# Kernel tuning notes

Hardware: AMD Instinct MI355X
Metric: run time of the kernel (lower is better)

Reference implementation:

```python
import jax, jax.numpy as jnp
import numpy as np

B, T, C = 2, 2048, 1024
H = 16
DH = C // H  # 64
DFF = 4 * C  # 4096
EPS = 1e-5


def layernorm(x, gamma, beta):
    # torch.var defaults to unbiased (ddof=1) -- replicate exactly
    m = jnp.mean(x, axis=-1, keepdims=True)
    v = jnp.var(x, axis=-1, ddof=1, keepdims=True)
    return (x - m) / jnp.sqrt(v + EPS) * gamma + beta


def setup_inputs() -> dict:
    key = jax.random.key(0)
    ks = jax.random.split(key, 12)
    s = 0.02
    return {
        "x": jax.random.normal(ks[0], (B, T, C), jnp.float32),
        "Wq": jax.random.normal(ks[1], (H, C, DH), jnp.float32) * s,
        "bq": jnp.zeros((H, DH), jnp.float32),
        "Wk": jax.random.normal(ks[2], (H, C, DH), jnp.float32) * s,
        "bk": jnp.zeros((H, DH), jnp.float32),
        "Wv": jax.random.normal(ks[3], (H, C, DH), jnp.float32) * s,
        "bv": jnp.zeros((H, DH), jnp.float32),
        "Wo": jax.random.normal(ks[4], (C, C), jnp.float32) * s,
        "bo": jnp.zeros((C,), jnp.float32),
        "gamma1": jnp.ones((C,), jnp.float32),
        "beta1": jnp.zeros((C,), jnp.float32),
        "gamma2": jnp.ones((C,), jnp.float32),
        "beta2": jnp.zeros((C,), jnp.float32),
        "W1": jax.random.normal(ks[5], (C, DFF), jnp.float32) * s,
        "b1": jnp.zeros((DFF,), jnp.float32),
        "W2": jax.random.normal(ks[6], (DFF, C), jnp.float32) * s,
        "b2": jnp.zeros((C,), jnp.float32),
    }


def reference(x, Wq, bq, Wk, bk, Wv, bv, Wo, bo,
              gamma1, beta1, gamma2, beta2, W1, b1, W2, b2):
    Tn = x.shape[1]
    # Block: x = ln1(x); x = x + attn(x); x = ln2(x); out = x + ffw(x)
    x = layernorm(x, gamma1, beta1)

    # per-head Q/K/V linears, stacked over heads: [B,T,C] x [H,C,Dh] -> [B,H,T,Dh]
    q = jnp.einsum('btc,hcd->bhtd', x, Wq) + bq[None, :, None, :]
    k = jnp.einsum('btc,hcd->bhtd', x, Wk) + bk[None, :, None, :]
    v = jnp.einsum('btc,hcd->bhtd', x, Wv) + bv[None, :, None, :]

    scale = DH ** -0.5
    scores = jnp.einsum('bhtd,bhsd->bhts', q, k) * scale  # [B,H,T,T]
    causal = jnp.tril(jnp.ones((Tn, Tn), dtype=bool))
    scores = jnp.where(causal, scores, -jnp.inf)
    alpha = jax.nn.softmax(scores, axis=-1)
    h = jnp.einsum('bhts,bhsd->bhtd', alpha, v)  # [B,H,T,Dh]
    h = jnp.transpose(h, (0, 2, 1, 3)).reshape(x.shape)  # concat heads -> [B,T,C]
    attn_out = h @ Wo + bo

    x = x + attn_out
    x = layernorm(x, gamma2, beta2)
    ffw = jax.nn.gelu(x @ W1 + b1, approximate=False) @ W2 + b2
    return x + ffw
```

## Files before the change

kernel.cpp:

```cpp
#include <hip/hip_runtime.h>

typedef unsigned short u16;
typedef unsigned int u32;
typedef __attribute__((ext_vector_type(8))) short bf16x8;
typedef __attribute__((ext_vector_type(4))) float f32x4;

#define AS1 __attribute__((address_space(1)))
#define AS3 __attribute__((address_space(3)))

__device__ __forceinline__ u16 f2bf(float f) {
  u32 u = __float_as_uint(f);
  u = (u + 0x7fffu + ((u >> 16) & 1u)) >> 16;
  return (u16)u;
}
__device__ __forceinline__ float bf2f(u16 v) { return __uint_as_float((u32)v << 16); }

__device__ __forceinline__ void gl16(const void* g, void* l) {
  __builtin_amdgcn_global_load_lds((AS1 void*)g, (AS3 void*)l, 16, 0, 0);
}

__device__ __forceinline__ float exp2a(float x) {
  float r;
  asm("v_exp_f32 %0, %1" : "=v"(r) : "v"(x));
  return r;
}
__device__ __forceinline__ u32 pk2(float lo, float hi) {
  u32 r;
  asm("v_cvt_pk_bf16_f32 %0, %1, %2" : "=v"(r) : "v"(lo), "v"(hi));
  return r;
}

#define BAR() __builtin_amdgcn_s_barrier()
#define LGKM0()                                         \
  do {                                                  \
    asm volatile("s_waitcnt lgkmcnt(0)" ::: "memory");  \
    __builtin_amdgcn_sched_barrier(0);                  \
  } while (0)
#define VMC0()                                          \
  do {                                                  \
    asm volatile("s_waitcnt vmcnt(0)" ::: "memory");    \
    __builtin_amdgcn_sched_barrier(0);                  \
  } while (0)

__global__ __launch_bounds__(256) void ln_kernel(const float* __restrict__ in,
                                                 const float* __restrict__ gamma,
                                                 const float* __restrict__ beta,
                                                 u16* __restrict__ obf,
                                                 float* __restrict__ of32) {
  const int row = blockIdx.x;
  const int tid = threadIdx.x;
  const float* xr = in + (long)row * 1024;
  float4 v = *(const float4*)(xr + tid * 4);
  float s = v.x + v.y + v.z + v.w;
  float sq = v.x * v.x + v.y * v.y + v.z * v.z + v.w * v.w;
#pragma unroll
  for (int off = 1; off < 64; off <<= 1) {
    s += __shfl_xor(s, off);
    sq += __shfl_xor(sq, off);
  }
  __shared__ float rs[4], rq[4];
  const int w = tid >> 6, lane = tid & 63;
  if (lane == 0) { rs[w] = s; rq[w] = sq; }
  __syncthreads();
  s = rs[0] + rs[1] + rs[2] + rs[3];
  sq = rq[0] + rq[1] + rq[2] + rq[3];
  const float mean = s * (1.0f / 1024.0f);
  const float var = (sq - 1024.0f * mean * mean) * (1.0f / 1023.0f);
  const float rstd = rsqrtf(var + 1e-5f);
  float4 g4 = *(const float4*)(gamma + tid * 4);
  float4 b4 = *(const float4*)(beta + tid * 4);
  float o0 = (v.x - mean) * rstd * g4.x + b4.x;
  float o1 = (v.y - mean) * rstd * g4.y + b4.y;
  float o2 = (v.z - mean) * rstd * g4.z + b4.z;
  float o3 = (v.w - mean) * rstd * g4.w + b4.w;
  *(float4*)(of32 + (long)row * 1024 + tid * 4) = make_float4(o0, o1, o2, o3);
  ushort4 ub;
  ub.x = f2bf(o0); ub.y = f2bf(o1); ub.z = f2bf(o2); ub.w = f2bf(o3);
  *(ushort4*)(obf + (long)row * 1024 + tid * 4) = ub;
}

__global__ __launch_bounds__(256) void ln2_fused_kernel(
    const u16* __restrict__ p0, const u16* __restrict__ p1,
    const float* __restrict__ bo, const float* __restrict__ xn,
    const float* __restrict__ gamma, const float* __restrict__ beta,
    u16* __restrict__ obf, float* __restrict__ of32) {
  const int row = blockIdx.x;
  const int tid = threadIdx.x;
  const long i4 = (long)row * 1024 + tid * 4;
  ushort4 a0 = *(const ushort4*)(p0 + i4);
  ushort4 a1 = *(const ushort4*)(p1 + i4);
  float4 xv = *(const float4*)(xn + i4);
  float4 bv = *(const float4*)(bo + tid * 4);
  float y0 = bf2f(a0.x) + bf2f(a1.x) + bv.x + xv.x;
  float y1 = bf2f(a0.y) + bf2f(a1.y) + bv.y + xv.y;
  float y2 = bf2f(a0.z) + bf2f(a1.z) + bv.z + xv.z;
  float y3 = bf2f(a0.w) + bf2f(a1.w) + bv.w + xv.w;
  float s = y0 + y1 + y2 + y3;
  float sq = y0 * y0 + y1 * y1 + y2 * y2 + y3 * y3;
#pragma unroll
  for (int off = 1; off < 64; off <<= 1) {
    s += __shfl_xor(s, off);
    sq += __shfl_xor(sq, off);
  }
  __shared__ float rs[4], rq[4];
  const int w = tid >> 6, lane = tid & 63;
  if (lane == 0) { rs[w] = s; rq[w] = sq; }
  __syncthreads();
  s = rs[0] + rs[1] + rs[2] + rs[3];
  sq = rq[0] + rq[1] + rq[2] + rq[3];
  const float mean = s * (1.0f / 1024.0f);
  const float var = (sq - 1024.0f * mean * mean) * (1.0f / 1023.0f);
  const float rstd = rsqrtf(var + 1e-5f);
  float4 g4 = *(const float4*)(gamma + tid * 4);
  float4 b4 = *(const float4*)(beta + tid * 4);
  float o0 = (y0 - mean) * rstd * g4.x + b4.x;
  float o1 = (y1 - mean) * rstd * g4.y + b4.y;
  float o2 = (y2 - mean) * rstd * g4.z + b4.z;
  float o3 = (y3 - mean) * rstd * g4.w + b4.w;
  *(float4*)(of32 + i4) = make_float4(o0, o1, o2, o3);
  ushort4 ub;
  ub.x = f2bf(o0); ub.y = f2bf(o1); ub.z = f2bf(o2); ub.w = f2bf(o3);
  *(ushort4*)(obf + i4) = ub;
}

__global__ __launch_bounds__(256) void wtrans_kernel(const float* __restrict__ in,
                                                     u16* __restrict__ out,
                                                     int R, int C, int in_rs,
                                                     long in_batch, long out_batch) {
  __shared__ float tile[32][33];
  const float* ip = in + (long)blockIdx.z * in_batch;
  u16* op = out + (long)blockIdx.z * out_batch;
  const int c0 = blockIdx.x * 32, r0 = blockIdx.y * 32;
  const int tx = threadIdx.x, ty = threadIdx.y;
#pragma unroll
  for (int i = 0; i < 4; ++i)
    tile[ty + i * 8][tx] = ip[(long)(r0 + ty + i * 8) * in_rs + c0 + tx];
  __syncthreads();
#pragma unroll
  for (int i = 0; i < 4; ++i)
    op[(long)(c0 + ty + i * 8) * R + r0 + tx] = f2bf(tile[tx][ty + i * 8]);
}

__device__ __forceinline__ void mfma_phase(f32x4 acc[8][4], const bf16x8 af[4][2],
                                           const bf16x8 bf[2][2], int mq, int nq) {
#pragma unroll
  for (int mf = 0; mf < 4; ++mf)
#pragma unroll
    for (int nf = 0; nf < 2; ++nf)
#pragma unroll
      for (int kh = 0; kh < 2; ++kh)
        acc[mq * 4 + mf][nq * 2 + nf] = __builtin_amdgcn_mfma_f32_16x16x32_bf16(
            af[mf][kh], bf[nf][kh], acc[mq * 4 + mf][nq * 2 + nf], 0, 0, 0);
}

#define STGA(BUFX)                                          \
  do {                                                      \
    gl16(pA0, Asm + (BUFX) * 16384 + tid * 8);              \
    gl16(pA1, Asm + (BUFX) * 16384 + 4096 + tid * 8);       \
    gl16(pA2, Asm + (BUFX) * 16384 + 8192 + tid * 8);       \
    gl16(pA3, Asm + (BUFX) * 16384 + 12288 + tid * 8);      \
  } while (0)
#define STGB(BUFX)                                          \
  do {                                                      \
    gl16(pB0, Bsm + (BUFX) * 16384 + tid * 8);              \
    gl16(pB1, Bsm + (BUFX) * 16384 + 4096 + tid * 8);       \
    gl16(pB2, Bsm + (BUFX) * 16384 + 8192 + tid * 8);       \
    gl16(pB3, Bsm + (BUFX) * 16384 + 12288 + tid * 8);      \
  } while (0)
#define ADVA() do { pA0 += 64; pA1 += 64; pA2 += 64; pA3 += 64; } while (0)
#define ADVB() do { pB0 += 64; pB1 += 64; pB2 += 64; pB3 += 64; } while (0)

#define RD(arr, off) (*(const bf16x8*)((arr) + (off)))

#define KTILE2(BUF, T)                                                       \
  do {                                                                       \
    bf16x8 af[4][2], bv0[2][2], bv1[2][2];                                   \
    _Pragma("unroll") for (int mf = 0; mf < 4; ++mf)                         \
        _Pragma("unroll") for (int kh = 0; kh < 2; ++kh)                     \
            af[mf][kh] = RD(Asm, aO[mf][kh] + (BUF) * 16384);                \
    _Pragma("unroll") for (int nf = 0; nf < 2; ++nf)                         \
        _Pragma("unroll") for (int kh = 0; kh < 2; ++kh) {                   \
      bv0[nf][kh] = RD(Bsm, bO[nf][kh] + (BUF) * 16384);                     \
      bv1[nf][kh] = RD(Bsm, bO[nf][kh] + (BUF) * 16384 + 2048);              \
    }                                                                        \
    if ((T) + 1 < nk) { STGA((BUF) ^ 1); STGB((BUF) ^ 1); }                  \
    LGKM0();                                                                 \
    mfma_phase(acc, af, bv0, 0, 0);                                          \
    mfma_phase(acc, af, bv1, 0, 1);                                          \
    _Pragma("unroll") for (int mf = 0; mf < 4; ++mf)                         \
        _Pragma("unroll") for (int kh = 0; kh < 2; ++kh)                     \
            af[mf][kh] = RD(Asm, aO[mf][kh] + (BUF) * 16384 + 4096);         \
    LGKM0();                                                                 \
    mfma_phase(acc, af, bv0, 1, 0);                                          \
    mfma_phase(acc, af, bv1, 1, 1);                                          \
    if ((T) + 1 < nk) VMC0();                                                \
    BAR();                                                                   \
  } while (0)

template <int EPI>
__global__ __launch_bounds__(512, 2) void gemm8_kernel(
    const u16* __restrict__ A, const u16* __restrict__ Bt,
    int lda, int ldb, int M, int N, int nk,
    const float* bias0, const float* bias1, const float* bias2,
    void* out0, void* out1) {
  __shared__ __align__(16) u16 Asm[4 * 8192];
  __shared__ __align__(16) u16 Bsm[4 * 8192];
  const int tid = threadIdx.x;
  const int lane = tid & 63, w = tid >> 6;
  const int wm = w >> 2, wn = w & 3;
  const int q15 = lane & 15, g = lane >> 4;

  const int nbx = gridDim.x, nby = gridDim.y;
  const int nwg = nbx * nby * gridDim.z;
  int lid = blockIdx.x + nbx * (blockIdx.y + nby * blockIdx.z);
  lid = (lid & 7) * (nwg >> 3) + (lid >> 3);
  const int bx = lid % nbx;
  const int rest = lid / nbx;
  const int by = rest % nby;
  const int bz = rest / nby;

  const long m0 = (long)bx * 256;
  const long n0 = (long)by * 256;
  const long koff = (long)bz * (long)nk * 64;
  const u16* Ab = A + m0 * lda + koff;
  const u16* Bb = Bt + n0 * ldb + koff;

  const int jr = tid >> 3;
  const int js = ((tid & 7) ^ (jr & 7)) * 8;
  const u16* pA0 = Ab + (long)jr * lda + js;
  const u16* pA1 = pA0 + (long)64 * lda;
  const u16* pA2 = pA0 + (long)128 * lda;
  const u16* pA3 = pA0 + (long)192 * lda;
  const u16* pB0 = Bb + (long)jr * ldb + js;
  const u16* pB1 = pB0 + (long)64 * ldb;
  const u16* pB2 = pB0 + (long)128 * ldb;
  const u16* pB3 = pB0 + (long)192 * ldb;

  int aO[4][2], bO[2][2];
#pragma unroll
  for (int mf = 0; mf < 4; ++mf)
#pragma unroll
    for (int kh = 0; kh < 2; ++kh) {
      const int rh = mf * 16 + q15;
      aO[mf][kh] = wm * 8192 + rh * 64 + (((kh * 4 + g) ^ (rh & 7)) * 8);
    }
  const int brow = (wn & 1) * 64;
#pragma unroll
  for (int nf = 0; nf < 2; ++nf)
#pragma unroll
    for (int kh = 0; kh < 2; ++kh) {
      const int rh = brow + nf * 16 + q15;
      bO[nf][kh] = (wn >> 1) * 8192 + rh * 64 + (((kh * 4 + g) ^ (rh & 7)) * 8);
    }

  f32x4 acc[8][4];
  f32x4 zero4 = {0.f, 0.f, 0.f, 0.f};
#pragma unroll
  for (int mi = 0; mi < 8; ++mi)
#pragma unroll
    for (int ni = 0; ni < 4; ++ni) acc[mi][ni] = zero4;

  STGA(0);
  STGB(0);
  ADVA();
  ADVB();
  VMC0();
  BAR();

  for (int tt = 0; tt < nk; tt += 2) {
    KTILE2(0, tt);
    ADVA(); ADVB();
    KTILE2(1, tt + 1);
    ADVA(); ADVB();
  }

#pragma unroll
  for (int mi = 0; mi < 8; ++mi) {
#pragma unroll
    for (int ni = 0; ni < 4; ++ni) {
      const long mbase = m0 + wm * 128 + (mi >> 2) * 64 + (mi & 3) * 16 + 4 * g;
      const long n = n0 + wn * 64 + (ni >> 1) * 32 + (ni & 1) * 16 + q15;
      f32x4 a = acc[mi][ni];
      if constexpr (EPI == 0) {
        const int sel = (int)(n >> 10);
        const int nn = (int)(n & 1023);
        const float* bp = sel == 0 ? bias0 : (sel == 1 ? bias1 : bias2);
        const float bb2 = bp[nn];
        if (sel < 2) {
          const float sc = (sel == 0) ? 0.18033688011112043f : 1.0f;
          u16* qkp = (u16*)out0;
#pragma unroll
          for (int r = 0; r < 4; ++r)
            qkp[(mbase + r) * 2048 + n] = f2bf((a[r] + bb2) * sc);
        } else {
          const int bI = (int)(mbase >> 11);
          const int t = (int)(mbase & 2047);
          const int hh = nn >> 6, dh = nn & 63;
          ushort4 pk;
          pk.x = f2bf(a[0] + bb2); pk.y = f2bf(a[1] + bb2);
          pk.z = f2bf(a[2] + bb2); pk.w = f2bf(a[3] + bb2);
          *(ushort4*)((u16*)out1 + ((long)((bI * 16 + hh) * 64 + dh)) * 2048 + t) = pk;
        }
      } else if constexpr (EPI == 2) {
        u16* gp = (u16*)out0;
        const float bb2 = bias0[(int)n];
#pragma unroll
        for (int r = 0; r < 4; ++r) {
          const float xg = a[r] + bb2;
          const float ge = 0.5f * xg * (1.0f + erff(xg * 0.70710678118f));
          gp[(mbase + r) * N + n] = f2bf(ge);
        }
      } else {
        u16* pp = (u16*)out0 + (long)bz * M * N;
#pragma unroll
        for (int r = 0; r < 4; ++r) pp[(mbase + r) * N + n] = f2bf(a[r]);
      }
    }
  }
}

__global__ __launch_bounds__(256) void ffn2_reduce_kernel(const u16* __restrict__ p,
                                                          const float* __restrict__ b2,
                                                          const float* __restrict__ yn,
                                                          float* __restrict__ out) {
  const long i4 = ((long)blockIdx.x * 256 + threadIdx.x) * 4;
  ushort4 p0 = *(const ushort4*)(p + i4);
  ushort4 p1 = *(const ushort4*)(p + 4194304 + i4);
  ushort4 p2 = *(const ushort4*)(p + 8388608 + i4);
  ushort4 p3 = *(const ushort4*)(p + 12582912 + i4);
  float4 rr = *(const float4*)(yn + i4);
  const int nn = (int)(i4 & 1023);
  float4 bb = *(const float4*)(b2 + nn);
  float4 o;
  o.x = bf2f(p0.x) + bf2f(p1.x) + bf2f(p2.x) + bf2f(p3.x) + bb.x + rr.x;
  o.y = bf2f(p0.y) + bf2f(p1.y) + bf2f(p2.y) + bf2f(p3.y) + bb.y + rr.y;
  o.z = bf2f(p0.z) + bf2f(p1.z) + bf2f(p2.z) + bf2f(p3.z) + bb.z + rr.z;
  o.w = bf2f(p0.w) + bf2f(p1.w) + bf2f(p2.w) + bf2f(p3.w) + bb.w + rr.w;
  *(float4*)(out + i4) = o;
}

__global__ __launch_bounds__(256, 2) void gemm_wo_kernel(const u16* __restrict__ A,
                                                         const u16* __restrict__ Bt,
                                                         u16* __restrict__ part) {
  __shared__ __align__(16) u16 Asm[128 * 64];
  __shared__ __align__(16) u16 Bsm[128 * 64];
  const int tid = threadIdx.x;
  const int lane = tid & 63, w = tid >> 6;
  const int wm = w >> 1, wn = w & 1;
  const int q = lane & 15, g = lane >> 4;
  const long m0 = (long)blockIdx.x * 128;
  const long n0 = (long)blockIdx.y * 128;
  const int bz = blockIdx.z;
  const long koff = (long)bz * 512;

  f32x4 zero4 = {0.f, 0.f, 0.f, 0.f};
  f32x4 acc[4][4];
#pragma unroll
  for (int mi = 0; mi < 4; ++mi)
#pragma unroll
    for (int ni = 0; ni < 4; ++ni) acc[mi][ni] = zero4;

  for (int ks = 0; ks < 8; ++ks) {
    __syncthreads();
    const u16* ga = A + m0 * 1024 + koff + ks * 64;
    const u16* gb = Bt + n0 * 1024 + koff + ks * 64;
    const int base = w * 256;
#pragma unroll
    for (int i = 0; i < 4; ++i) {
      const int idx = base + i * 64 + lane;
      const int row = idx >> 3;
      const int lg = (idx & 7) ^ (row & 7);
      gl16(ga + (long)row * 1024 + lg * 8, Asm + (long)(base + i * 64) * 8);
    }
#pragma unroll
    for (int i = 0; i < 4; ++i) {
      const int idx = base + i * 64 + lane;
      const int row = idx >> 3;
      const int lg = (idx & 7) ^ (row & 7);
      gl16(gb + (long)row * 1024 + lg * 8, Bsm + (long)(base + i * 64) * 8);
    }
    __syncthreads();
#pragma unroll
    for (int half = 0; half < 2; ++half) {
      bf16x8 af[4], bfv[4];
#pragma unroll
      for (int mi = 0; mi < 4; ++mi) {
        const int row = wm * 64 + mi * 16 + q;
        const int ph = (half * 4 + g) ^ (row & 7);
        af[mi] = *(const bf16x8*)(Asm + row * 64 + ph * 8);
      }
#pragma unroll
      for (int ni = 0; ni < 4; ++ni) {
        const int row = wn * 64 + ni * 16 + q;
        const int ph = (half * 4 + g) ^ (row & 7);
        bfv[ni] = *(const bf16x8*)(Bsm + row * 64 + ph * 8);
      }
#pragma unroll
      for (int mi = 0; mi < 4; ++mi)
#pragma unroll
        for (int ni = 0; ni < 4; ++ni)
          acc[mi][ni] = __builtin_amdgcn_mfma_f32_16x16x32_bf16(af[mi], bfv[ni],
                                                                acc[mi][ni], 0, 0, 0);
    }
  }
  u16* pp = part + (long)bz * 4096 * 1024;
#pragma unroll
  for (int mi = 0; mi < 4; ++mi) {
#pragma unroll
    for (int ni = 0; ni < 4; ++ni) {
      const long mbase = m0 + wm * 64 + mi * 16 + 4 * g;
      const long n = n0 + wn * 64 + ni * 16 + q;
      f32x4 a = acc[mi][ni];
#pragma unroll
      for (int r = 0; r < 4; ++r) pp[(mbase + r) * 1024 + n] = f2bf(a[r]);
    }
  }
}

__device__ __forceinline__ void attn_stage(const u16* kbase, const u16* vtb, int kb,
                                           u16* Kd, u16* Vd, int tid) {
#pragma unroll
  for (int it = 0; it < 2; ++it) {
    const int j = it * 256 + tid;
    const int row = j >> 3;
    const int lg = (j & 7) ^ (row & 7);
    gl16(kbase + (long)(kb * 64 + row) * 2048 + lg * 8, Kd + j * 8);
    gl16(vtb + (long)row * 2048 + kb * 64 + lg * 8, Vd + j * 8);
  }
}

__device__ __forceinline__ void softmax_slab(const f32x4 st[4], bool diag, int qrow,
                                             int kb, int g, int q15,
                                             float& m2, float& l, u16* prow,
                                             float al[4]) {
  float sv[4][4];
  float rmax = -1e30f;
#pragma unroll
  for (int sub = 0; sub < 4; ++sub)
#pragma unroll
    for (int r = 0; r < 4; ++r) {
      float s_ = st[sub][r];
      if (diag) {
        const int key = kb * 64 + sub * 16 + 4 * g + r;
        s_ = (key > qrow) ? -1e30f : s_;
      }
      sv[sub][r] = s_;
      rmax = fmaxf(rmax, s_);
    }
  rmax = fmaxf(rmax, __shfl_xor(rmax, 16));
  rmax = fmaxf(rmax, __shfl_xor(rmax, 32));
  const float mnew = fmaxf(m2, rmax);
  const float alpha = exp2a(m2 - mnew);
  float psum = 0.f;
#pragma unroll
  for (int sub = 0; sub < 4; ++sub) {
    const float p0 = exp2a(sv[sub][0] - mnew);
    const float p1 = exp2a(sv[sub][1] - mnew);
    const float p2 = exp2a(sv[sub][2] - mnew);
    const float p3 = exp2a(sv[sub][3] - mnew);
    uint2 u;
    u.x = pk2(p0, p1);
    u.y = pk2(p2, p3);
    *(uint2*)(prow + sub * 16 + 4 * g) = u;
    psum += (p0 + p1) + (p2 + p3);
  }
  psum += __shfl_xor(psum, 16);
  psum += __shfl_xor(psum, 32);
  l = l * alpha + psum;
  m2 = mnew;
#pragma unroll
  for (int r = 0; r < 4; ++r) al[r] = __shfl(alpha, 4 * g + r);
}

__global__ __launch_bounds__(256, 2) void attn_kernel(const u16* __restrict__ qk,
                                                      const u16* __restrict__ vT,
                                                      u16* __restrict__ o) {
  __shared__ __align__(16) u16 Ksm[2][64 * 64];
  __shared__ __align__(16) u16 Vsm[2][64 * 64];
  __shared__ __align__(16) u16 Psm[8][16][72];
  const int lid = blockIdx.x;
  const int xcd = lid & 7, s6 = lid >> 3;
  const int b2 = (s6 >> 4) & 3, xr = s6 & 15;
  const int qs = (b2 & 2) ? (15 - xr) : xr;
  const int bh = xcd + 8 * b2;
  const int b = bh >> 4, h = bh & 15;
  const int tid = threadIdx.x, lane = tid & 63, w = tid >> 6;
  const int q15 = lane & 15, g = lane >> 4;
  const u16* qbase = qk + (long)b * 2048 * 2048 + h * 64;
  const u16* kbase = qbase + 1024;
  const u16* vtb = vT + (long)bh * 64 * 2048;
  f32x4 zero4 = {0.f, 0.f, 0.f, 0.f};

  const int r0 = qs * 128 + w * 16 + q15;
  bf16x8 qa[2][2];
  qa[0][0] = *(const bf16x8*)(qbase + (long)r0 * 2048 + g * 8);
  qa[0][1] = *(const bf16x8*)(qbase + (long)r0 * 2048 + 32 + g * 8);
  qa[1][0] = *(const bf16x8*)(qbase + (long)(r0 + 64) * 2048 + g * 8);
  qa[1][1] = *(const bf16x8*)(qbase + (long)(r0 + 64) * 2048 + 32 + g * 8);

  f32x4 oa0[4], oa1[4];
#pragma unroll
  for (int dv = 0; dv < 4; ++dv) { oa0[dv] = zero4; oa1[dv] = zero4; }
  float m20 = -1e30f, l0 = 0.f, m21 = -1e30f, l1 = 0.f;
  const int kbmax = 2 * qs + 1;

  attn_stage(kbase, vtb, 0, Ksm[0], Vsm[0], tid);
  VMC0();
  __syncthreads();

  for (int kb = 0; kb <= kbmax; ++kb) {
    const int buf = kb & 1;
    if (kb < kbmax) attn_stage(kbase, vtb, kb + 1, Ksm[buf ^ 1], Vsm[buf ^ 1], tid);
    const u16* Kb = Ksm[buf];
    const u16* Vb = Vsm[buf];
    const bool s0on = (kb <= 2 * qs);
    f32x4 st0[4], st1[4];
#pragma unroll
    for (int sub = 0; sub < 4; ++sub) {
      const int row = sub * 16 + q15;
      const bf16x8 ka0 = *(const bf16x8*)(Kb + row * 64 + ((g ^ (row & 7)) * 8));
      const bf16x8 ka1 = *(const bf16x8*)(Kb + row * 64 + (((4 + g) ^ (row & 7)) * 8));
      f32x4 z = zero4;
      z = __builtin_amdgcn_mfma_f32_16x16x32_bf16(ka0, qa[1][0], z, 0, 0, 0);
      z = __builtin_amdgcn_mfma_f32_16x16x32_bf16(ka1, qa[1][1], z, 0, 0, 0);
      st1[sub] = z;
      if (s0on) {
        f32x4 z0 = zero4;
        z0 = __builtin_amdgcn_mfma_f32_16x16x32_bf16(ka0, qa[0][0], z0, 0, 0, 0);
        z0 = __builtin_amdgcn_mfma_f32_16x16x32_bf16(ka1, qa[0][1], z0, 0, 0, 0);
        st0[sub] = z0;
      }
    }
    float al0[4], al1[4];
    if (s0on)
      softmax_slab(st0, kb == 2 * qs, r0, kb, g, q15, m20, l0, &Psm[w * 2][q15][0], al0);
    softmax_slab(st1, kb == 2 * qs + 1, r0 + 64, kb, g, q15, m21, l1,
                 &Psm[w * 2 + 1][q15][0], al1);
    if (s0on)
#pragma unroll
      for (int dv = 0; dv < 4; ++dv) {
        oa0[dv][0] *= al0[0]; oa0[dv][1] *= al0[1];
        oa0[dv][2] *= al0[2]; oa0[dv][3] *= al0[3];
      }
#pragma unroll
    for (int dv = 0; dv < 4; ++dv) {
      oa1[dv][0] *= al1[0]; oa1[dv][1] *= al1[1];
      oa1[dv][2] *= al1[2]; oa1[dv][3] *= al1[3];
    }
    LGKM0();
#pragma unroll
    for (int half = 0; half < 2; ++half) {
      const bf16x8 pa0 = *(const bf16x8*)(&Psm[w * 2][q15][half * 32 + 8 * g]);
      const bf16x8 pa1 = *(const bf16x8*)(&Psm[w * 2 + 1][q15][half * 32 + 8 * g]);
#pragma unroll
      for (int dv = 0; dv < 4; ++dv) {
        const int row = dv * 16 + q15;
        const bf16x8 vb = *(const bf16x8*)(Vb + row * 64 + (((half * 4 + g) ^ (row & 7)) * 8));
        if (s0on) oa0[dv] = __builtin_amdgcn_mfma_f32_16x16x32_bf16(pa0, vb, oa0[dv], 0, 0, 0);
        oa1[dv] = __builtin_amdgcn_mfma_f32_16x16x32_bf16(pa1, vb, oa1[dv], 0, 0, 0);
      }
    }
    VMC0();
    __syncthreads();
  }
  const float li0 = 1.0f / l0, li1 = 1.0f / l1;
  float v0[4], v1[4];
#pragma unroll
  for (int r = 0; r < 4; ++r) {
    v0[r] = __shfl(li0, 4 * g + r);
    v1[r] = __shfl(li1, 4 * g + r);
  }
  const int tok0 = b * 2048 + qs * 128 + w * 16;
#pragma unroll
  for (int dv = 0; dv < 4; ++dv)
#pragma unroll
    for (int r = 0; r < 4; ++r) {
      o[(long)(tok0 + 4 * g + r) * 1024 + h * 64 + dv * 16 + q15] =
          f2bf(oa0[dv][r] * v0[r]);
      o[(long)(tok0 + 64 + 4 * g + r) * 1024 + h * 64 + dv * 16 + q15] =
          f2bf(oa1[dv][r] * v1[r]);
    }
}

extern "C" void kernel_launch(void* const* d_in, const int* in_sizes, int n_in,
                              void* d_out, int out_size, void* d_ws, size_t ws_size,
                              hipStream_t stream) {
  (void)in_sizes; (void)n_in; (void)out_size; (void)ws_size;
  const float* x  = (const float*)d_in[0];
  const float* Wq = (const float*)d_in[1];
  const float* bq = (const float*)d_in[2];
  const float* Wk = (const float*)d_in[3];
  const float* bk = (const float*)d_in[4];
  const float* Wv = (const float*)d_in[5];
  const float* bv = (const float*)d_in[6];
  const float* Wo = (const float*)d_in[7];
  const float* bo = (const float*)d_in[8];
  const float* g1 = (const float*)d_in[9];
  const float* be1 = (const float*)d_in[10];
  const float* g2 = (const float*)d_in[11];
  const float* be2 = (const float*)d_in[12];
  const float* W1 = (const float*)d_in[13];
  const float* b1 = (const float*)d_in[14];
  const float* W2 = (const float*)d_in[15];
  const float* b2 = (const float*)d_in[16];

  char* ws = (char*)d_ws;
  u16*   xn_bf = (u16*)  (ws + 0);
  float* xn_f  = (float*)(ws + 8388608);
  u16*   WqkvT = (u16*)  (ws + 25165824);
  u16*   WoT   = (u16*)  (ws + 31457280);
  u16*   W1T   = (u16*)  (ws + 33554432);
  u16*   W2T   = (u16*)  (ws + 41943040);
  u16*   qkb   = (u16*)  (ws + 50331648);
  u16*   vTb   = (u16*)  (ws + 67108864);
  u16*   ah    = (u16*)  (ws + 75497472);
  u16*   pwo0  = (u16*)  (ws + 50331648);
  u16*   pwo1  = (u16*)  (ws + 58720256);
  u16*   gbuf  = (u16*)  (ws + 50331648);
  u16*   part  = (u16*)  (ws + 0);
  u16*   yn_bf = (u16*)  (ws + 83886080);
  float* yn_f  = (float*)(ws + 92274688);

  dim3 tb(32, 8), b256(256), b512(512);
  wtrans_kernel<<<dim3(2, 32, 16), tb, 0, stream>>>(Wq, WqkvT,            1024, 64, 64, 65536l, 65536l);
  wtrans_kernel<<<dim3(2, 32, 16), tb, 0, stream>>>(Wk, WqkvT + 1048576,  1024, 64, 64, 65536l, 65536l);
  wtrans_kernel<<<dim3(2, 32, 16), tb, 0, stream>>>(Wv, WqkvT + 2097152,  1024, 64, 64, 65536l, 65536l);
  wtrans_kernel<<<dim3(32, 32, 1),  tb, 0, stream>>>(Wo, WoT, 1024, 1024, 1024, 0l, 0l);
  wtrans_kernel<<<dim3(128, 32, 1), tb, 0, stream>>>(W1, W1T, 1024, 4096, 4096, 0l, 0l);
  wtrans_kernel<<<dim3(32, 128, 1), tb, 0, stream>>>(W2, W2T, 4096, 1024, 1024, 0l, 0l);
  ln_kernel<<<dim3(4096), b256, 0, stream>>>(x, g1, be1, xn_bf, xn_f);
  gemm8_kernel<0><<<dim3(16, 12, 1), b512, 0, stream>>>(xn_bf, WqkvT, 1024, 1024,
                                                        4096, 3072, 16, bq, bk, bv, qkb, vTb);
  attn_kernel<<<dim3(512), b256, 0, stream>>>(qkb, vTb, ah);
  gemm_wo_kernel<<<dim3(32, 8, 2), b256, 0, stream>>>(ah, WoT, pwo0);
  ln2_fused_kernel<<<dim3(4096), b256, 0, stream>>>(pwo0, pwo1, bo, xn_f, g2, be2,
                                                    yn_bf, yn_f);
  gemm8_kernel<2><<<dim3(16, 16, 1), b512, 0, stream>>>(yn_bf, W1T, 1024, 1024,
                                                        4096, 4096, 16, b1, nullptr, nullptr, gbuf, nullptr);
  gemm8_kernel<4><<<dim3(16, 4, 4), b512, 0, stream>>>(gbuf, W2T, 4096, 4096,
                                                       4096, 1024, 16, nullptr, nullptr, nullptr, part, nullptr);
  ffn2_reduce_kernel<<<dim3(4096), b256, 0, stream>>>(part, b2, yn_f, (float*)d_out);
}
```

Before: 239.4 us.

## Use 128-tile GEMM for QKV and load attention K/V directly into registers

The QKV projection moves from the 256x256 8-wave GEMM to a generalized 128x128 4-wave GEMM with the QKV epilogue, launching more workgroups (768 instead of 192) for better CU fill. The attention kernel drops its LDS double-buffering of K and V tiles and the per-iteration barrier, loading K and V fragments straight from global memory into registers instead. This removes LDS staging and synchronisation but relies on L2/cache for the repeated K/V reads, with less latency hiding and more uncoalesced global traffic.

```diff
diff --git a/kernel.cpp b/kernel.cpp
--- a/kernel.cpp
+++ b/kernel.cpp
@@ -201,8 +201,7 @@
 __global__ __launch_bounds__(512, 2) void gemm8_kernel(
     const u16* __restrict__ A, const u16* __restrict__ Bt,
     int lda, int ldb, int M, int N, int nk,
-    const float* bias0, const float* bias1, const float* bias2,
-    void* out0, void* out1) {
+    const float* bias0, void* out0) {
   __shared__ __align__(16) u16 Asm[4 * 8192];
   __shared__ __align__(16) u16 Bsm[4 * 8192];
   const int tid = threadIdx.x;
@@ -281,27 +280,7 @@
       const long mbase = m0 + wm * 128 + (mi >> 2) * 64 + (mi & 3) * 16 + 4 * g;
       const long n = n0 + wn * 64 + (ni >> 1) * 32 + (ni & 1) * 16 + q15;
       f32x4 a = acc[mi][ni];
-      if constexpr (EPI == 0) {
-        const int sel = (int)(n >> 10);
-        const int nn = (int)(n & 1023);
-        const float* bp = sel == 0 ? bias0 : (sel == 1 ? bias1 : bias2);
-        const float bb2 = bp[nn];
-        if (sel < 2) {
-          const float sc = (sel == 0) ? 0.18033688011112043f : 1.0f;
-          u16* qkp = (u16*)out0;
-#pragma unroll
-          for (int r = 0; r < 4; ++r)
-            qkp[(mbase + r) * 2048 + n] = f2bf((a[r] + bb2) * sc);
-        } else {
-          const int bI = (int)(mbase >> 11);
-          const int t = (int)(mbase & 2047);
-          const int hh = nn >> 6, dh = nn & 63;
-          ushort4 pk;
-          pk.x = f2bf(a[0] + bb2); pk.y = f2bf(a[1] + bb2);
-          pk.z = f2bf(a[2] + bb2); pk.w = f2bf(a[3] + bb2);
-          *(ushort4*)((u16*)out1 + ((long)((bI * 16 + hh) * 64 + dh)) * 2048 + t) = pk;
-        }
-      } else if constexpr (EPI == 2) {
+      if constexpr (EPI == 2) {
         u16* gp = (u16*)out0;
         const float bb2 = bias0[(int)n];
 #pragma unroll
@@ -339,9 +318,12 @@
   *(float4*)(out + i4) = o;
 }
 
-__global__ __launch_bounds__(256, 2) void gemm_wo_kernel(const u16* __restrict__ A,
-                                                         const u16* __restrict__ Bt,
-                                                         u16* __restrict__ part) {
+template <int EPI>
+__global__ __launch_bounds__(256, 2) void gemm128_kernel(
+    const u16* __restrict__ A, const u16* __restrict__ Bt,
+    int K, int nk,
+    const float* bias0, const float* bias1, const float* bias2,
+    void* out0, void* out1) {
   __shared__ __align__(16) u16 Asm[128 * 64];
   __shared__ __align__(16) u16 Bsm[128 * 64];
   const int tid = threadIdx.x;
@@ -351,7 +333,7 @@
   const long m0 = (long)blockIdx.x * 128;
   const long n0 = (long)blockIdx.y * 128;
   const int bz = blockIdx.z;
-  const long koff = (long)bz * 512;
+  const long koff = (long)bz * (long)nk * 64;
 
   f32x4 zero4 = {0.f, 0.f, 0.f, 0.f};
   f32x4 acc[4][4];
@@ -360,24 +342,24 @@
 #pragma unroll
     for (int ni = 0; ni < 4; ++ni) acc[mi][ni] = zero4;
 
-  for (int ks = 0; ks < 8; ++ks) {
+  for (int ks = 0; ks < nk; ++ks) {
     __syncthreads();
-    const u16* ga = A + m0 * 1024 + koff + ks * 64;
-    const u16* gb = Bt + n0 * 1024 + koff + ks * 64;
+    const u16* ga = A + m0 * K + koff + ks * 64;
+    const u16* gb = Bt + n0 * K + koff + ks * 64;
     const int base = w * 256;
 #pragma unroll
     for (int i = 0; i < 4; ++i) {
       const int idx = base + i * 64 + lane;
       const int row = idx >> 3;
       const int lg = (idx & 7) ^ (row & 7);
-      gl16(ga + (long)row * 1024 + lg * 8, Asm + (long)(base + i * 64) * 8);
+      gl16(ga + (long)row * K + lg * 8, Asm + (long)(base + i * 64) * 8);
     }
 #pragma unroll
     for (int i = 0; i < 4; ++i) {
       const int idx = base + i * 64 + lane;
       const int row = idx >> 3;
       const int lg = (idx & 7) ^ (row & 7);
-      gl16(gb + (long)row * 1024 + lg * 8, Bsm + (long)(base + i * 64) * 8);
+      gl16(gb + (long)row * K + lg * 8, Bsm + (long)(base + i * 64) * 8);
     }
     __syncthreads();
 #pragma unroll
@@ -403,7 +385,6 @@
                                                                 acc[mi][ni], 0, 0, 0);
     }
   }
-  u16* pp = part + (long)bz * 4096 * 1024;
 #pragma unroll
   for (int mi = 0; mi < 4; ++mi) {
 #pragma unroll
@@ -411,21 +392,32 @@
       const long mbase = m0 + wm * 64 + mi * 16 + 4 * g;
       const long n = n0 + wn * 64 + ni * 16 + q;
       f32x4 a = acc[mi][ni];
-#pragma unroll
-      for (int r = 0; r < 4; ++r) pp[(mbase + r) * 1024 + n] = f2bf(a[r]);
-    }
-  }
-}
-
-__device__ __forceinline__ void attn_stage(const u16* kbase, const u16* vtb, int kb,
-                                           u16* Kd, u16* Vd, int tid) {
-#pragma unroll
-  for (int it = 0; it < 2; ++it) {
-    const int j = it * 256 + tid;
-    const int row = j >> 3;
-    const int lg = (j & 7) ^ (row & 7);
-    gl16(kbase + (long)(kb * 64 + row) * 2048 + lg * 8, Kd + j * 8);
-    gl16(vtb + (long)row * 2048 + kb * 64 + lg * 8, Vd + j * 8);
+      if constexpr (EPI == 0) {
+        const int sel = (int)(n >> 10);
+        const int nn = (int)(n & 1023);
+        const float* bp = sel == 0 ? bias0 : (sel == 1 ? bias1 : bias2);
+        const float bb2 = bp[nn];
+        if (sel < 2) {
+          const float sc = (sel == 0) ? 0.18033688011112043f : 1.0f;
+          u16* qkp = (u16*)out0;
+#pragma unroll
+          for (int r = 0; r < 4; ++r)
+            qkp[(mbase + r) * 2048 + n] = f2bf((a[r] + bb2) * sc);
+        } else {
+          const int bI = (int)(mbase >> 11);
+          const int t = (int)(mbase & 2047);
+          const int hh = nn >> 6, dh = nn & 63;
+          ushort4 pk;
+          pk.x = f2bf(a[0] + bb2); pk.y = f2bf(a[1] + bb2);
+          pk.z = f2bf(a[2] + bb2); pk.w = f2bf(a[3] + bb2);
+          *(ushort4*)((u16*)out1 + ((long)((bI * 16 + hh) * 64 + dh)) * 2048 + t) = pk;
+        }
+      } else {
+        u16* pp = (u16*)out0 + (long)bz * 4096 * 1024;
+#pragma unroll
+        for (int r = 0; r < 4; ++r) pp[(mbase + r) * 1024 + n] = f2bf(a[r]);
+      }
+    }
   }
 }
 
@@ -475,8 +467,6 @@
 __global__ __launch_bounds__(256, 2) void attn_kernel(const u16* __restrict__ qk,
                                                       const u16* __restrict__ vT,
                                                       u16* __restrict__ o) {
-  __shared__ __align__(16) u16 Ksm[2][64 * 64];
-  __shared__ __align__(16) u16 Vsm[2][64 * 64];
   __shared__ __align__(16) u16 Psm[8][16][72];
   const int lid = blockIdx.x;
   const int xcd = lid & 7, s6 = lid >> 3;
@@ -504,33 +494,37 @@
   float m20 = -1e30f, l0 = 0.f, m21 = -1e30f, l1 = 0.f;
   const int kbmax = 2 * qs + 1;
 
-  attn_stage(kbase, vtb, 0, Ksm[0], Vsm[0], tid);
-  VMC0();
-  __syncthreads();
-
   for (int kb = 0; kb <= kbmax; ++kb) {
-    const int buf = kb & 1;
-    if (kb < kbmax) attn_stage(kbase, vtb, kb + 1, Ksm[buf ^ 1], Vsm[buf ^ 1], tid);
-    const u16* Kb = Ksm[buf];
-    const u16* Vb = Vsm[buf];
     const bool s0on = (kb <= 2 * qs);
+    bf16x8 ka[4][2];
+#pragma unroll
+    for (int sub = 0; sub < 4; ++sub)
+#pragma unroll
+      for (int kh = 0; kh < 2; ++kh)
+        ka[sub][kh] = *(const bf16x8*)(kbase +
+            (long)(kb * 64 + sub * 16 + q15) * 2048 + kh * 32 + g * 8);
     f32x4 st0[4], st1[4];
 #pragma unroll
     for (int sub = 0; sub < 4; ++sub) {
-      const int row = sub * 16 + q15;
-      const bf16x8 ka0 = *(const bf16x8*)(Kb + row * 64 + ((g ^ (row & 7)) * 8));
-      const bf16x8 ka1 = *(const bf16x8*)(Kb + row * 64 + (((4 + g) ^ (row & 7)) * 8));
       f32x4 z = zero4;
-      z = __builtin_amdgcn_mfma_f32_16x16x32_bf16(ka0, qa[1][0], z, 0, 0, 0);
-      z = __builtin_amdgcn_mfma_f32_16x16x32_bf16(ka1, qa[1][1], z, 0, 0, 0);
+      z = __builtin_amdgcn_mfma_f32_16x16x32_bf16(ka[sub][0], qa[1][0], z, 0, 0, 0);
+      z = __builtin_amdgcn_mfma_f32_16x16x32_bf16(ka[sub][1], qa[1][1], z, 0, 0, 0);
       st1[sub] = z;
       if (s0on) {
         f32x4 z0 = zero4;
-        z0 = __builtin_amdgcn_mfma_f32_16x16x32_bf16(ka0, qa[0][0], z0, 0, 0, 0);
-        z0 = __builtin_amdgcn_mfma_f32_16x16x32_bf16(ka1, qa[0][1], z0, 0, 0, 0);
+        z0 = __builtin_amdgcn_mfma_f32_16x16x32_bf16(ka[sub][0], qa[0][0], z0, 0, 0, 0);
+        z0 = __builtin_amdgcn_mfma_f32_16x16x32_bf16(ka[sub][1], qa[0][1], z0, 0, 0, 0);
         st0[sub] = z0;
       }
     }
+    bf16x8 vb[2][4];
+#pragma unroll
+    for (int half = 0; half < 2; ++half)
+#pragma unroll
+      for (int dv = 0; dv < 4; ++dv)
+        vb[half][dv] = *(const bf16x8*)(vtb +
+            (long)(dv * 16 + q15) * 2048 + kb * 64 + half * 32 + g * 8);
+
     float al0[4], al1[4];
     if (s0on)
       softmax_slab(st0, kb == 2 * qs, r0, kb, g, q15, m20, l0, &Psm[w * 2][q15][0], al0);
@@ -554,14 +548,10 @@
       const bf16x8 pa1 = *(const bf16x8*)(&Psm[w * 2 + 1][q15][half * 32 + 8 * g]);
 #pragma unroll
       for (int dv = 0; dv < 4; ++dv) {
-        const int row = dv * 16 + q15;
-        const bf16x8 vb = *(const bf16x8*)(Vb + row * 64 + (((half * 4 + g) ^ (row & 7)) * 8));
-        if (s0on) oa0[dv] = __builtin_amdgcn_mfma_f32_16x16x32_bf16(pa0, vb, oa0[dv], 0, 0, 0);
-        oa1[dv] = __builtin_amdgcn_mfma_f32_16x16x32_bf16(pa1, vb, oa1[dv], 0, 0, 0);
-      }
-    }
-    VMC0();
-    __syncthreads();
+        if (s0on) oa0[dv] = __builtin_amdgcn_mfma_f32_16x16x32_bf16(pa0, vb[half][dv], oa0[dv], 0, 0, 0);
+        oa1[dv] = __builtin_amdgcn_mfma_f32_16x16x32_bf16(pa1, vb[half][dv], oa1[dv], 0, 0, 0);
+      }
+    }
   }
   const float li0 = 1.0f / l0, li1 = 1.0f / l1;
   float v0[4], v1[4];
@@ -629,15 +619,16 @@
   wtrans_kernel<<<dim3(128, 32, 1), tb, 0, stream>>>(W1, W1T, 1024, 4096, 4096, 0l, 0l);
   wtrans_kernel<<<dim3(32, 128, 1), tb, 0, stream>>>(W2, W2T, 4096, 1024, 1024, 0l, 0l);
   ln_kernel<<<dim3(4096), b256, 0, stream>>>(x, g1, be1, xn_bf, xn_f);
-  gemm8_kernel<0><<<dim3(16, 12, 1), b512, 0, stream>>>(xn_bf, WqkvT, 1024, 1024,
-                                                        4096, 3072, 16, bq, bk, bv, qkb, vTb);
+  gemm128_kernel<0><<<dim3(32, 24, 1), b256, 0, stream>>>(xn_bf, WqkvT, 1024, 16,
+                                                          bq, bk, bv, qkb, vTb);
   attn_kernel<<<dim3(512), b256, 0, stream>>>(qkb, vTb, ah);
-  gemm_wo_kernel<<<dim3(32, 8, 2), b256, 0, stream>>>(ah, WoT, pwo0);
+  gemm128_kernel<5><<<dim3(32, 8, 2), b256, 0, stream>>>(ah, WoT, 1024, 8,
+                                                         nullptr, nullptr, nullptr, pwo0, nullptr);
   ln2_fused_kernel<<<dim3(4096), b256, 0, stream>>>(pwo0, pwo1, bo, xn_f, g2, be2,
                                                     yn_bf, yn_f);
   gemm8_kernel<2><<<dim3(16, 16, 1), b512, 0, stream>>>(yn_bf, W1T, 1024, 1024,
-                                                        4096, 4096, 16, b1, nullptr, nullptr, gbuf, nullptr);
+                                                        4096, 4096, 16, b1, gbuf);
   gemm8_kernel<4><<<dim3(16, 4, 4), b512, 0, stream>>>(gbuf, W2T, 4096, 4096,
-                                                       4096, 1024, 16, nullptr, nullptr, nullptr, part, nullptr);
+                                                       4096, 1024, 16, nullptr, part);
   ffn2_reduce_kernel<<<dim3(4096), b256, 0, stream>>>(part, b2, yn_f, (float*)d_out);
 }
```

After: 256.1 us. +7.0%, slower.

## Replace 256x256 double-buffered GEMM with generic 128x128 single-buffer GEMM

Applied to the files above, without the earlier changes.

Removes the 512-thread 256x256 double-buffered gemm8 kernel and generalizes the simpler 128x128 Wo GEMM into a templated gemm128 kernel with per-call epilogues. The QKV, FFN1 and FFN2 GEMMs now run with smaller tiles, more blocks and a single LDS buffer with synchronous barriers. This gives more workgroups and likely higher occupancy, but loses load/compute overlap and cuts data reuse per tile.

```diff
diff --git a/kernel.cpp b/kernel.cpp
--- a/kernel.cpp
+++ b/kernel.cpp
@@ -30,7 +30,6 @@
   return r;
 }
 
-#define BAR() __builtin_amdgcn_s_barrier()
 #define LGKM0()                                         \
   do {                                                  \
     asm volatile("s_waitcnt lgkmcnt(0)" ::: "memory");  \
@@ -141,184 +140,6 @@
     op[(long)(c0 + ty + i * 8) * R + r0 + tx] = f2bf(tile[tx][ty + i * 8]);
 }
 
-__device__ __forceinline__ void mfma_phase(f32x4 acc[8][4], const bf16x8 af[4][2],
-                                           const bf16x8 bf[2][2], int mq, int nq) {
-#pragma unroll
-  for (int mf = 0; mf < 4; ++mf)
-#pragma unroll
-    for (int nf = 0; nf < 2; ++nf)
-#pragma unroll
-      for (int kh = 0; kh < 2; ++kh)
-        acc[mq * 4 + mf][nq * 2 + nf] = __builtin_amdgcn_mfma_f32_16x16x32_bf16(
-            af[mf][kh], bf[nf][kh], acc[mq * 4 + mf][nq * 2 + nf], 0, 0, 0);
-}
-
-#define STGA(BUFX)                                          \
-  do {                                                      \
-    gl16(pA0, Asm + (BUFX) * 16384 + tid * 8);              \
-    gl16(pA1, Asm + (BUFX) * 16384 + 4096 + tid * 8);       \
-    gl16(pA2, Asm + (BUFX) * 16384 + 8192 + tid * 8);       \
-    gl16(pA3, Asm + (BUFX) * 16384 + 12288 + tid * 8);      \
-  } while (0)
-#define STGB(BUFX)                                          \
-  do {                                                      \
-    gl16(pB0, Bsm + (BUFX) * 16384 + tid * 8);              \
-    gl16(pB1, Bsm + (BUFX) * 16384 + 4096 + tid * 8);       \
-    gl16(pB2, Bsm + (BUFX) * 16384 + 8192 + tid * 8);       \
-    gl16(pB3, Bsm + (BUFX) * 16384 + 12288 + tid * 8);      \
-  } while (0)
-#define ADVA() do { pA0 += 64; pA1 += 64; pA2 += 64; pA3 += 64; } while (0)
-#define ADVB() do { pB0 += 64; pB1 += 64; pB2 += 64; pB3 += 64; } while (0)
-
-#define RD(arr, off) (*(const bf16x8*)((arr) + (off)))
-
-#define KTILE2(BUF, T)                                                       \
-  do {                                                                       \
-    bf16x8 af[4][2], bv0[2][2], bv1[2][2];                                   \
-    _Pragma("unroll") for (int mf = 0; mf < 4; ++mf)                         \
-        _Pragma("unroll") for (int kh = 0; kh < 2; ++kh)                     \
-            af[mf][kh] = RD(Asm, aO[mf][kh] + (BUF) * 16384);                \
-    _Pragma("unroll") for (int nf = 0; nf < 2; ++nf)                         \
-        _Pragma("unroll") for (int kh = 0; kh < 2; ++kh) {                   \
-      bv0[nf][kh] = RD(Bsm, bO[nf][kh] + (BUF) * 16384);                     \
-      bv1[nf][kh] = RD(Bsm, bO[nf][kh] + (BUF) * 16384 + 2048);              \
-    }                                                                        \
-    if ((T) + 1 < nk) { STGA((BUF) ^ 1); STGB((BUF) ^ 1); }                  \
-    LGKM0();                                                                 \
-    mfma_phase(acc, af, bv0, 0, 0);                                          \
-    mfma_phase(acc, af, bv1, 0, 1);                                          \
-    _Pragma("unroll") for (int mf = 0; mf < 4; ++mf)                         \
-        _Pragma("unroll") for (int kh = 0; kh < 2; ++kh)                     \
-            af[mf][kh] = RD(Asm, aO[mf][kh] + (BUF) * 16384 + 4096);         \
-    LGKM0();                                                                 \
-    mfma_phase(acc, af, bv0, 1, 0);                                          \
-    mfma_phase(acc, af, bv1, 1, 1);                                          \
-    if ((T) + 1 < nk) VMC0();                                                \
-    BAR();                                                                   \
-  } while (0)
-
-template <int EPI>
-__global__ __launch_bounds__(512, 2) void gemm8_kernel(
-    const u16* __restrict__ A, const u16* __restrict__ Bt,
-    int lda, int ldb, int M, int N, int nk,
-    const float* bias0, const float* bias1, const float* bias2,
-    void* out0, void* out1) {
-  __shared__ __align__(16) u16 Asm[4 * 8192];
-  __shared__ __align__(16) u16 Bsm[4 * 8192];
-  const int tid = threadIdx.x;
-  const int lane = tid & 63, w = tid >> 6;
-  const int wm = w >> 2, wn = w & 3;
-  const int q15 = lane & 15, g = lane >> 4;
-
-  const int nbx = gridDim.x, nby = gridDim.y;
-  const int nwg = nbx * nby * gridDim.z;
-  int lid = blockIdx.x + nbx * (blockIdx.y + nby * blockIdx.z);
-  lid = (lid & 7) * (nwg >> 3) + (lid >> 3);
-  const int bx = lid % nbx;
-  const int rest = lid / nbx;
-  const int by = rest % nby;
-  const int bz = rest / nby;
-
-  const long m0 = (long)bx * 256;
-  const long n0 = (long)by * 256;
-  const long koff = (long)bz * (long)nk * 64;
-  const u16* Ab = A + m0 * lda + koff;
-  const u16* Bb = Bt + n0 * ldb + koff;
-
-  const int jr = tid >> 3;
-  const int js = ((tid & 7) ^ (jr & 7)) * 8;
-  const u16* pA0 = Ab + (long)jr * lda + js;
-  const u16* pA1 = pA0 + (long)64 * lda;
-  const u16* pA2 = pA0 + (long)128 * lda;
-  const u16* pA3 = pA0 + (long)192 * lda;
-  const u16* pB0 = Bb + (long)jr * ldb + js;
-  const u16* pB1 = pB0 + (long)64 * ldb;
-  const u16* pB2 = pB0 + (long)128 * ldb;
-  const u16* pB3 = pB0 + (long)192 * ldb;
-
-  int aO[4][2], bO[2][2];
-#pragma unroll
-  for (int mf = 0; mf < 4; ++mf)
-#pragma unroll
-    for (int kh = 0; kh < 2; ++kh) {
-      const int rh = mf * 16 + q15;
-      aO[mf][kh] = wm * 8192 + rh * 64 + (((kh * 4 + g) ^ (rh & 7)) * 8);
-    }
-  const int brow = (wn & 1) * 64;
-#pragma unroll
-  for (int nf = 0; nf < 2; ++nf)
-#pragma unroll
-    for (int kh = 0; kh < 2; ++kh) {
-      const int rh = brow + nf * 16 + q15;
-      bO[nf][kh] = (wn >> 1) * 8192 + rh * 64 + (((kh * 4 + g) ^ (rh & 7)) * 8);
-    }
-
-  f32x4 acc[8][4];
-  f32x4 zero4 = {0.f, 0.f, 0.f, 0.f};
-#pragma unroll
-  for (int mi = 0; mi < 8; ++mi)
-#pragma unroll
-    for (int ni = 0; ni < 4; ++ni) acc[mi][ni] = zero4;
-
-  STGA(0);
-  STGB(0);
-  ADVA();
-  ADVB();
-  VMC0();
-  BAR();
-
-  for (int tt = 0; tt < nk; tt += 2) {
-    KTILE2(0, tt);
-    ADVA(); ADVB();
-    KTILE2(1, tt + 1);
-    ADVA(); ADVB();
-  }
-
-#pragma unroll
-  for (int mi = 0; mi < 8; ++mi) {
-#pragma unroll
-    for (int ni = 0; ni < 4; ++ni) {
-      const long mbase = m0 + wm * 128 + (mi >> 2) * 64 + (mi & 3) * 16 + 4 * g;
-      const long n = n0 + wn * 64 + (ni >> 1) * 32 + (ni & 1) * 16 + q15;
-      f32x4 a = acc[mi][ni];
-      if constexpr (EPI == 0) {
-        const int sel = (int)(n >> 10);
-        const int nn = (int)(n & 1023);
-        const float* bp = sel == 0 ? bias0 : (sel == 1 ? bias1 : bias2);
-        const float bb2 = bp[nn];
-        if (sel < 2) {
-          const float sc = (sel == 0) ? 0.18033688011112043f : 1.0f;
-          u16* qkp = (u16*)out0;
-#pragma unroll
-          for (int r = 0; r < 4; ++r)
-            qkp[(mbase + r) * 2048 + n] = f2bf((a[r] + bb2) * sc);
-        } else {
-          const int bI = (int)(mbase >> 11);
-          const int t = (int)(mbase & 2047);
-          const int hh = nn >> 6, dh = nn & 63;
-          ushort4 pk;
-          pk.x = f2bf(a[0] + bb2); pk.y = f2bf(a[1] + bb2);
-          pk.z = f2bf(a[2] + bb2); pk.w = f2bf(a[3] + bb2);
-          *(ushort4*)((u16*)out1 + ((long)((bI * 16 + hh) * 64 + dh)) * 2048 + t) = pk;
-        }
-      } else if constexpr (EPI == 2) {
-        u16* gp = (u16*)out0;
-        const float bb2 = bias0[(int)n];
-#pragma unroll
-        for (int r = 0; r < 4; ++r) {
-          const float xg = a[r] + bb2;
-          const float ge = 0.5f * xg * (1.0f + erff(xg * 0.70710678118f));
-          gp[(mbase + r) * N + n] = f2bf(ge);
-        }
-      } else {
-        u16* pp = (u16*)out0 + (long)bz * M * N;
-#pragma unroll
-        for (int r = 0; r < 4; ++r) pp[(mbase + r) * N + n] = f2bf(a[r]);
-      }
-    }
-  }
-}
-
 __global__ __launch_bounds__(256) void ffn2_reduce_kernel(const u16* __restrict__ p,
                                                           const float* __restrict__ b2,
                                                           const float* __restrict__ yn,
@@ -339,9 +160,12 @@
   *(float4*)(out + i4) = o;
 }
 
-__global__ __launch_bounds__(256, 2) void gemm_wo_kernel(const u16* __restrict__ A,
-                                                         const u16* __restrict__ Bt,
-                                                         u16* __restrict__ part) {
+template <int EPI>
+__global__ __launch_bounds__(256, 2) void gemm128_kernel(
+    const u16* __restrict__ A, const u16* __restrict__ Bt,
+    int K, int nk, int N,
+    const float* bias0, const float* bias1, const float* bias2,
+    void* out0, void* out1) {
   __shared__ __align__(16) u16 Asm[128 * 64];
   __shared__ __align__(16) u16 Bsm[128 * 64];
   const int tid = threadIdx.x;
@@ -351,7 +175,7 @@
   const long m0 = (long)blockIdx.x * 128;
   const long n0 = (long)blockIdx.y * 128;
   const int bz = blockIdx.z;
-  const long koff = (long)bz * 512;
+  const long koff = (long)bz * (long)nk * 64;
 
   f32x4 zero4 = {0.f, 0.f, 0.f, 0.f};
   f32x4 acc[4][4];
@@ -360,24 +184,24 @@
 #pragma unroll
     for (int ni = 0; ni < 4; ++ni) acc[mi][ni] = zero4;
 
-  for (int ks = 0; ks < 8; ++ks) {
+  for (int ks = 0; ks < nk; ++ks) {
     __syncthreads();
-    const u16* ga = A + m0 * 1024 + koff + ks * 64;
-    const u16* gb = Bt + n0 * 1024 + koff + ks * 64;
+    const u16* ga = A + m0 * K + koff + ks * 64;
+    const u16* gb = Bt + n0 * K + koff + ks * 64;
     const int base = w * 256;
 #pragma unroll
     for (int i = 0; i < 4; ++i) {
       const int idx = base + i * 64 + lane;
       const int row = idx >> 3;
       const int lg = (idx & 7) ^ (row & 7);
-      gl16(ga + (long)row * 1024 + lg * 8, Asm + (long)(base + i * 64) * 8);
+      gl16(ga + (long)row * K + lg * 8, Asm + (long)(base + i * 64) * 8);
     }
 #pragma unroll
     for (int i = 0; i < 4; ++i) {
       const int idx = base + i * 64 + lane;
       const int row = idx >> 3;
       const int lg = (idx & 7) ^ (row & 7);
-      gl16(gb + (long)row * 1024 + lg * 8, Bsm + (long)(base + i * 64) * 8);
+      gl16(gb + (long)row * K + lg * 8, Bsm + (long)(base + i * 64) * 8);
     }
     __syncthreads();
 #pragma unroll
@@ -403,7 +227,6 @@
                                                                 acc[mi][ni], 0, 0, 0);
     }
   }
-  u16* pp = part + (long)bz * 4096 * 1024;
 #pragma unroll
   for (int mi = 0; mi < 4; ++mi) {
 #pragma unroll
@@ -411,8 +234,40 @@
       const long mbase = m0 + wm * 64 + mi * 16 + 4 * g;
       const long n = n0 + wn * 64 + ni * 16 + q;
       f32x4 a = acc[mi][ni];
-#pragma unroll
-      for (int r = 0; r < 4; ++r) pp[(mbase + r) * 1024 + n] = f2bf(a[r]);
+      if constexpr (EPI == 0) {
+        const int sel = (int)(n >> 10);
+        const int nn = (int)(n & 1023);
+        const float* bp = sel == 0 ? bias0 : (sel == 1 ? bias1 : bias2);
+        const float bb2 = bp[nn];
+        if (sel < 2) {
+          const float sc = (sel == 0) ? 0.18033688011112043f : 1.0f;
+          u16* qkp = (u16*)out0;
+#pragma unroll
+          for (int r = 0; r < 4; ++r)
+            qkp[(mbase + r) * 2048 + n] = f2bf((a[r] + bb2) * sc);
+        } else {
+          const int bI = (int)(mbase >> 11);
+          const int t = (int)(mbase & 2047);
+          const int hh = nn >> 6, dh = nn & 63;
+          ushort4 pk;
+          pk.x = f2bf(a[0] + bb2); pk.y = f2bf(a[1] + bb2);
+          pk.z = f2bf(a[2] + bb2); pk.w = f2bf(a[3] + bb2);
+          *(ushort4*)((u16*)out1 + ((long)((bI * 16 + hh) * 64 + dh)) * 2048 + t) = pk;
+        }
+      } else if constexpr (EPI == 2) {
+        u16* gp = (u16*)out0;
+        const float bb2 = bias0[(int)n];
+#pragma unroll
+        for (int r = 0; r < 4; ++r) {
+          const float xg = a[r] + bb2;
+          const float ge = 0.5f * xg * (1.0f + erff(xg * 0.70710678118f));
+          gp[(mbase + r) * N + n] = f2bf(ge);
+        }
+      } else {
+        u16* pp = (u16*)out0 + (long)bz * 4096 * 1024;
+#pragma unroll
+        for (int r = 0; r < 4; ++r) pp[(mbase + r) * 1024 + n] = f2bf(a[r]);
+      }
     }
   }
 }
@@ -621,7 +476,7 @@
   u16*   yn_bf = (u16*)  (ws + 83886080);
   float* yn_f  = (float*)(ws + 92274688);
 
-  dim3 tb(32, 8), b256(256), b512(512);
+  dim3 tb(32, 8), b256(256);
   wtrans_kernel<<<dim3(2, 32, 16), tb, 0, stream>>>(Wq, WqkvT,            1024, 64, 64, 65536l, 65536l);
   wtrans_kernel<<<dim3(2, 32, 16), tb, 0, stream>>>(Wk, WqkvT + 1048576,  1024, 64, 64, 65536l, 65536l);
   wtrans_kernel<<<dim3(2, 32, 16), tb, 0, stream>>>(Wv, WqkvT + 2097152,  1024, 64, 64, 65536l, 65536l);
@@ -629,15 +484,16 @@
   wtrans_kernel<<<dim3(128, 32, 1), tb, 0, stream>>>(W1, W1T, 1024, 4096, 4096, 0l, 0l);
   wtrans_kernel<<<dim3(32, 128, 1), tb, 0, stream>>>(W2, W2T, 4096, 1024, 1024, 0l, 0l);
   ln_kernel<<<dim3(4096), b256, 0, stream>>>(x, g1, be1, xn_bf, xn_f);
-  gemm8_kernel<0><<<dim3(16, 12, 1), b512, 0, stream>>>(xn_bf, WqkvT, 1024, 1024,
-                                                        4096, 3072, 16, bq, bk, bv, qkb, vTb);
+  gemm128_kernel<0><<<dim3(32, 24, 1), b256, 0, stream>>>(xn_bf, WqkvT, 1024, 16, 3072,
+                                                          bq, bk, bv, qkb, vTb);
   attn_kernel<<<dim3(512), b256, 0, stream>>>(qkb, vTb, ah);
-  gemm_wo_kernel<<<dim3(32, 8, 2), b256, 0, stream>>>(ah, WoT, pwo0);
+  gemm128_kernel<5><<<dim3(32, 8, 2), b256, 0, stream>>>(ah, WoT, 1024, 8, 1024,
+                                                         nullptr, nullptr, nullptr, pwo0, nullptr);
   ln2_fused_kernel<<<dim3(4096), b256, 0, stream>>>(pwo0, pwo1, bo, xn_f, g2, be2,
                                                     yn_bf, yn_f);
-  gemm8_kernel<2><<<dim3(16, 16, 1), b512, 0, stream>>>(yn_bf, W1T, 1024, 1024,
-                                                        4096, 4096, 16, b1, nullptr, nullptr, gbuf, nullptr);
-  gemm8_kernel<4><<<dim3(16, 4, 4), b512, 0, stream>>>(gbuf, W2T, 4096, 4096,
-                                                       4096, 1024, 16, nullptr, nullptr, nullptr, part, nullptr);
+  gemm128_kernel<2><<<dim3(32, 32, 1), b256, 0, stream>>>(yn_bf, W1T, 1024, 16, 4096,
+                                                          b1, nullptr, nullptr, gbuf, nullptr);
+  gemm128_kernel<5><<<dim3(32, 8, 4), b256, 0, stream>>>(gbuf, W2T, 4096, 16, 1024,
+                                                         nullptr, nullptr, nullptr, part, nullptr);
   ffn2_reduce_kernel<<<dim3(4096), b256, 0, stream>>>(part, b2, yn_f, (float*)d_out);
 }
```

Result: faster. 229.1 us (-4.3%).
